# Kernel tuning notes

Measured on AMD Instinct MI355X. Metric: run time of the kernel, lower is better.

Reference implementation:

```python
import jax, jax.numpy as jnp
import numpy as np

ALIGN_SCALE = 3.0
UNIF_SCALE = 1.0
EPS = 1e-12  # torch F.normalize eps


def _normalize(x):
    n = jnp.linalg.norm(x, axis=-1, keepdims=True)
    return x / jnp.maximum(n, EPS)


def _unif_loss(a, b):
    # log(mean(exp(-2 * ||a_i - b_j||^2))) over all N*M pairs, fused via GEMM identity
    sq_a = jnp.sum(a * a, axis=1)  # [N]
    sq_b = jnp.sum(b * b, axis=1)  # [M]
    # squared distances: ||a||^2 + ||b||^2 - 2 a.b, clipped at 0 for numerics
    d2 = jnp.maximum(sq_a[:, None] + sq_b[None, :] - 2.0 * (a @ b.T), 0.0)  # [N, M]
    return jnp.log(jnp.mean(jnp.exp(-2.0 * d2)))


def setup_inputs() -> dict:
    key = jax.random.key(0)
    k1, k2 = jax.random.split(key)
    N, D = 8192, 512
    return {
        "image_embed": jax.random.normal(k1, (N, D), dtype=jnp.float32),
        "text_embed": jax.random.normal(k2, (N, D), dtype=jnp.float32),
    }


def reference(image_embed, text_embed):
    img = _normalize(image_embed)
    txt = _normalize(text_embed)
    # alignment: mean squared L2 between paired embeddings
    diff = img - txt
    align_loss = jnp.mean(jnp.sum(diff * diff, axis=1))
    # single device: gathered-all tensors equal the local tensors
    text_unif = _unif_loss(txt, txt)
    image_unif = _unif_loss(img, img)
    unif_loss = (text_unif + image_unif) / 2.0
    return ALIGN_SCALE * align_loss + UNIF_SCALE * unif_loss
```

## Files before the change

kernel.cpp:

```cpp
#include <hip/hip_runtime.h>
#include <hip/hip_bf16.h>


#define NROWS 8192
#define DBYTES 256
#define NBLK  1056
#define SCALE4 0x7B7B7B7B

typedef __attribute__((ext_vector_type(8)))  int   int8v;
typedef __attribute__((ext_vector_type(4)))  int   int4v;
typedef __attribute__((ext_vector_type(16))) float float16v;

__device__ inline void load_lds16(const void* g, void* l) {
    __builtin_amdgcn_global_load_lds(
        (const __attribute__((address_space(1))) void*)g,
        (__attribute__((address_space(3))) void*)l, 16, 0, 0);
}

__device__ inline int swz(int r) { return (r ^ (r >> 3)) & 7; }

__device__ inline unsigned fp4_code(float x) {
    const float a = fabsf(x);
    unsigned c = (a < 0.25f) ? 0u : (a < 0.75f) ? 1u : (a < 1.25f) ? 2u :
                 (a < 1.75f) ? 3u : (a < 2.5f)  ? 4u : (a < 3.5f)  ? 5u :
                 (a < 5.0f)  ? 6u : 7u;
    return c | ((__float_as_uint(x) >> 28) & 8u);
}

__global__ __launch_bounds__(256) void normalize_kernel(
    const float* __restrict__ img, const float* __restrict__ txt,
    int* __restrict__ nimg, int* __restrict__ ntxt,
    float* __restrict__ alignp,
    float* __restrict__ S)
{
    if (blockIdx.x == 0 && threadIdx.x < 64) S[threadIdx.x] = 0.0f;

    const int lane = threadIdx.x & 63;
    const int wave = threadIdx.x >> 6;
    const int row  = blockIdx.x * 4 + wave;

    const float4* pi = (const float4*)(img + (size_t)row * 512);
    const float4* pt = (const float4*)(txt + (size_t)row * 512);
    const float4 i0 = pi[2 * lane], i1 = pi[2 * lane + 1];
    const float4 t0 = pt[2 * lane], t1 = pt[2 * lane + 1];

    float ssi = i0.x*i0.x + i0.y*i0.y + i0.z*i0.z + i0.w*i0.w
              + i1.x*i1.x + i1.y*i1.y + i1.z*i1.z + i1.w*i1.w;
    float sst = t0.x*t0.x + t0.y*t0.y + t0.z*t0.z + t0.w*t0.w
              + t1.x*t1.x + t1.y*t1.y + t1.z*t1.z + t1.w*t1.w;
    float dot = i0.x*t0.x + i0.y*t0.y + i0.z*t0.z + i0.w*t0.w
              + i1.x*t1.x + i1.y*t1.y + i1.z*t1.z + i1.w*t1.w;

    #pragma unroll
    for (int off = 1; off < 64; off <<= 1) {
        ssi += __shfl_xor(ssi, off);
        sst += __shfl_xor(sst, off);
        dot += __shfl_xor(dot, off);
    }
    const float inv_i = 1.0f / fmaxf(sqrtf(ssi), 1e-12f);
    const float inv_t = 1.0f / fmaxf(sqrtf(sst), 1e-12f);
    const float si = 16.0f * inv_i;
    const float st = 16.0f * inv_t;

    unsigned wi = 0, wt = 0;
    wi |= fp4_code(i0.x * si)       | (fp4_code(i0.y * si) << 4)
       |  (fp4_code(i0.z * si) << 8)| (fp4_code(i0.w * si) << 12)
       |  (fp4_code(i1.x * si) <<16)| (fp4_code(i1.y * si) << 20)
       |  (fp4_code(i1.z * si) <<24)| (fp4_code(i1.w * si) << 28);
    wt |= fp4_code(t0.x * st)       | (fp4_code(t0.y * st) << 4)
       |  (fp4_code(t0.z * st) << 8)| (fp4_code(t0.w * st) << 12)
       |  (fp4_code(t1.x * st) <<16)| (fp4_code(t1.y * st) << 20)
       |  (fp4_code(t1.z * st) <<24)| (fp4_code(t1.w * st) << 28);

    nimg[row * 64 + lane] = (int)wi;
    ntxt[row * 64 + lane] = (int)wt;

    __shared__ float r4[4];
    if (lane == 0) r4[wave] = dot * inv_i * inv_t;
    __syncthreads();
    if (threadIdx.x == 0)
        alignp[blockIdx.x] = r4[0] + r4[1] + r4[2] + r4[3];
}

__global__ __launch_bounds__(512, 2) void gram_kernel(
    const unsigned char* __restrict__ A0,
    const unsigned char* __restrict__ A1,
    float* __restrict__ S)
{
    const int b = blockIdx.x;
    int I = (int)((65.0f - sqrtf(4225.0f - 4.0f * (float)b)) * 0.5f);
    while ((I + 1) * (64 - I) <= b) ++I;
    while (I * (65 - I) > b) --I;
    const int j = 2 * I + (b - I * (65 - I));

    const unsigned char* __restrict__ A = blockIdx.y ? A1 : A0;
    const int tid  = threadIdx.x;
    const int lane = tid & 63;
    const int wave = tid >> 6;
    const int wm = wave & 3;
    const int wn = wave >> 2;
    const int lr = lane & 31;
    const int h  = lane >> 5;

    const unsigned char* gA = A + (size_t)I * 256 * DBYTES;
    const unsigned char* gB = A + (size_t)j * 128 * DBYTES;

    __shared__ __align__(16) unsigned char ldsA[2][256 * 128];
    __shared__ __align__(16) unsigned char ldsB[2][128 * 128];

    float16v acc[2][2];
    #pragma unroll
    for (int a = 0; a < 2; ++a)
        #pragma unroll
        for (int c = 0; c < 2; ++c)
            #pragma unroll
            for (int r = 0; r < 16; ++r) acc[a][c][r] = 0.0f;

    #pragma unroll
    for (int s = 0; s < 2; ++s) {
        const int k0 = s * 128;
        #pragma unroll
        for (int rnd = 0; rnd < 4; ++rnd) {
            const int slot = rnd * 8192 + tid * 16;
            const int r    = slot >> 7;
            const int cp   = (slot >> 4) & 7;
            const int cl   = cp ^ swz(r);
            load_lds16(gA + (size_t)r * DBYTES + k0 + cl * 16, &ldsA[s][slot]);
        }
        #pragma unroll
        for (int rnd = 0; rnd < 2; ++rnd) {
            const int slot = rnd * 8192 + tid * 16;
            const int r    = slot >> 7;
            const int cp   = (slot >> 4) & 7;
            const int cl   = cp ^ swz(r);
            load_lds16(gB + (size_t)r * DBYTES + k0 + cl * 16, &ldsB[s][slot]);
        }
        __builtin_amdgcn_sched_barrier(0);
    }

    asm volatile("s_waitcnt vmcnt(6)" ::: "memory");
    __builtin_amdgcn_sched_barrier(0);
    __builtin_amdgcn_s_barrier();
    __builtin_amdgcn_sched_barrier(0);

    #pragma unroll
    for (int s = 0; s < 2; ++s) {
        #pragma unroll
        for (int kk = 0; kk < 4; ++kk) {
            const int c0 = kk * 2 + h;
            int8v av[2], bv[2];
            #pragma unroll
            for (int mt = 0; mt < 2; ++mt) {
                const int r = wm * 64 + mt * 32 + lr;
                *((int4v*)&av[mt]) =
                    *(const int4v*)&ldsA[s][r * 128 + (c0 ^ swz(r)) * 16];
                *((int4v*)&av[mt] + 1) = (int4v){0, 0, 0, 0};
            }
            #pragma unroll
            for (int nt = 0; nt < 2; ++nt) {
                const int r = wn * 64 + nt * 32 + lr;
                *((int4v*)&bv[nt]) =
                    *(const int4v*)&ldsB[s][r * 128 + (c0 ^ swz(r)) * 16];
                *((int4v*)&bv[nt] + 1) = (int4v){0, 0, 0, 0};
            }
            #pragma unroll
            for (int mt = 0; mt < 2; ++mt)
                #pragma unroll
                for (int nt = 0; nt < 2; ++nt)
                    acc[mt][nt] = __builtin_amdgcn_mfma_scale_f32_32x32x64_f8f6f4(
                        av[mt], bv[nt], acc[mt][nt],
                        4, 4,
                        0, SCALE4,
                        0, SCALE4);
        }
        if (s == 0) {
            asm volatile("s_waitcnt vmcnt(0)" ::: "memory");
            __builtin_amdgcn_s_barrier();
            __builtin_amdgcn_sched_barrier(0);
        }
    }

    const int r128 = 2 * I + (wm >> 1);
    const float wv = (j > r128) ? 2.0f : ((j == r128) ? 1.0f : 0.0f);
    float s = 0.0f;
    #pragma unroll
    for (int mt = 0; mt < 2; ++mt)
        #pragma unroll
        for (int nt = 0; nt < 2; ++nt)
            #pragma unroll
            for (int r2 = 0; r2 < 16; ++r2) {
                const float g = acc[mt][nt][r2];
                s += __expf(4.0f * fminf(g, 1.0f) - 4.0f);
            }
    s *= wv;
    #pragma unroll
    for (int off = 32; off; off >>= 1) s += __shfl_down(s, off);
    __shared__ float ps[8];
    if (lane == 0) ps[wave] = s;
    __syncthreads();
    if (tid == 0) {
        const float tot = ps[0] + ps[1] + ps[2] + ps[3]
                        + ps[4] + ps[5] + ps[6] + ps[7];
        atomicAdd(&S[blockIdx.y * 32 + (blockIdx.x & 31)], tot);
    }
}

__global__ __launch_bounds__(256) void finalize_kernel(
    const float* __restrict__ S,
    const float* __restrict__ alignp,
    float* __restrict__ out)
{
    const int tid = threadIdx.x;
    float a = 0.0f;
    #pragma unroll
    for (int k = 0; k < 8; ++k) a += alignp[tid + 256 * k];
    #pragma unroll
    for (int off = 32; off; off >>= 1) a += __shfl_down(a, off);
    __shared__ float r4[4];
    if ((tid & 63) == 0) r4[tid >> 6] = a;
    __syncthreads();
    if (tid == 0) {
        const double A = (double)r4[0] + r4[1] + r4[2] + r4[3];
        double si = 0.0, st = 0.0;
        for (int k = 0; k < 32; ++k) { si += S[k]; st += S[32 + k]; }
        const double align = 2.0 - 2.0 * A / (double)NROWS;
        const double n2 = (double)NROWS * (double)NROWS;
        const double unif = 0.5 * (log(si / n2) + log(st / n2));
        out[0] = (float)(3.0 * align + unif);
    }
}

extern "C" void kernel_launch(void* const* d_in, const int* in_sizes, int n_in,
                              void* d_out, int out_size, void* d_ws, size_t ws_size,
                              hipStream_t stream) {
    const float* img = (const float*)d_in[0];
    const float* txt = (const float*)d_in[1];
    char* ws = (char*)d_ws;
    int* nimg = (int*)ws;
    int* ntxt = (int*)(ws + (size_t)NROWS * DBYTES);
    float* S      = (float*)(ws + 2 * (size_t)NROWS * DBYTES);
    float* alignp = S + 64;

    normalize_kernel<<<NROWS / 4, 256, 0, stream>>>(img, txt, nimg, ntxt, alignp, S);
    dim3 grid(NBLK, 2);
    gram_kernel<<<grid, 512, 0, stream>>>((const unsigned char*)nimg,
                                          (const unsigned char*)ntxt, S);
    finalize_kernel<<<1, 256, 0, stream>>>(S, alignp, (float*)d_out);
}
```

Baseline: 120.9 us.

## Make gram kernel persistent with 128x128 triangular jobs and double-buffered prefetch

Replaces the 2112-block grid of 256x128 tiles with a persistent grid of 512 blocks of 256 threads. Each block loops over 128x128 upper-triangle jobs from both matrices, with the next K-half staged into LDS while the current one is computed. The diagonal tiles are now exactly triangular, so no half-wasted 256-row strips, and the per-block launch and prologue cost is hidden by the software pipeline. The trade-offs are smaller tiles with less reuse per load, a barrier every stage, and possible load imbalance since jobs don't divide evenly across blocks.

```diff
diff --git a/kernel.cpp b/kernel.cpp
--- a/kernel.cpp
+++ b/kernel.cpp
@@ -4,7 +4,9 @@
 
 #define NROWS 8192
 #define DBYTES 256
-#define NBLK  1056
+#define NTRI  2080
+#define NJOBS 4160
+#define GRAMBLK 512
 #define SCALE4 0x7B7B7B7B
 
 typedef __attribute__((ext_vector_type(8)))  int   int8v;
@@ -82,31 +84,68 @@
         alignp[blockIdx.x] = r4[0] + r4[1] + r4[2] + r4[3];
 }
 
-__global__ __launch_bounds__(512, 2) void gram_kernel(
+__device__ inline void decode_job(int t,
+        const unsigned char* __restrict__ A0,
+        const unsigned char* __restrict__ A1,
+        const unsigned char*& pA, const unsigned char*& pB,
+        float& w0, float& w1)
+{
+    const int m  = (t >= NTRI) ? 1 : 0;
+    const int tt = t - m * NTRI;
+    int i = (int)((129.0f - sqrtf(16641.0f - 8.0f * (float)tt)) * 0.5f);
+    while (64 * (i + 1) - ((i + 1) * i) / 2 <= tt) ++i;
+    while (64 * i - (i * (i - 1)) / 2 > tt) --i;
+    const int j = i + (tt - (64 * i - (i * (i - 1)) / 2));
+    const unsigned char* M = m ? A1 : A0;
+    pA = M + (size_t)i * 128 * DBYTES;
+    pB = M + (size_t)j * 128 * DBYTES;
+    const float w = (j > i) ? 2.0f : 1.0f;
+    w0 = m ? 0.0f : w;
+    w1 = m ? w : 0.0f;
+}
+
+__device__ inline void stage_tile(const unsigned char* __restrict__ pA,
+                                  const unsigned char* __restrict__ pB,
+                                  int k0, unsigned char* lA, unsigned char* lB,
+                                  int tid)
+{
+    #pragma unroll
+    for (int rnd = 0; rnd < 4; ++rnd) {
+        const int slot = rnd * 4096 + tid * 16;
+        const int r    = slot >> 7;
+        const int cp   = (slot >> 4) & 7;
+        const int cl   = cp ^ swz(r);
+        load_lds16(pA + (size_t)r * DBYTES + k0 + cl * 16, lA + slot);
+    }
+    #pragma unroll
+    for (int rnd = 0; rnd < 4; ++rnd) {
+        const int slot = rnd * 4096 + tid * 16;
+        const int r    = slot >> 7;
+        const int cp   = (slot >> 4) & 7;
+        const int cl   = cp ^ swz(r);
+        load_lds16(pB + (size_t)r * DBYTES + k0 + cl * 16, lB + slot);
+    }
+}
+
+__global__ __launch_bounds__(256, 2) void gram_kernel(
     const unsigned char* __restrict__ A0,
     const unsigned char* __restrict__ A1,
     float* __restrict__ S)
 {
-    const int b = blockIdx.x;
-    int I = (int)((65.0f - sqrtf(4225.0f - 4.0f * (float)b)) * 0.5f);
-    while ((I + 1) * (64 - I) <= b) ++I;
-    while (I * (65 - I) > b) --I;
-    const int j = 2 * I + (b - I * (65 - I));
-
-    const unsigned char* __restrict__ A = blockIdx.y ? A1 : A0;
     const int tid  = threadIdx.x;
     const int lane = tid & 63;
     const int wave = tid >> 6;
-    const int wm = wave & 3;
-    const int wn = wave >> 2;
+    const int wm = wave & 1, wn = wave >> 1;
     const int lr = lane & 31;
     const int h  = lane >> 5;
-
-    const unsigned char* gA = A + (size_t)I * 256 * DBYTES;
-    const unsigned char* gB = A + (size_t)j * 128 * DBYTES;
-
-    __shared__ __align__(16) unsigned char ldsA[2][256 * 128];
+    const int b  = blockIdx.x;
+
+    __shared__ __align__(16) unsigned char ldsA[2][128 * 128];
     __shared__ __align__(16) unsigned char ldsB[2][128 * 128];
+    __shared__ float ps[4][2];
+
+    const int J = (NJOBS - 1 - b) / GRAMBLK + 1;
+    const int U = 2 * J;
 
     float16v acc[2][2];
     #pragma unroll
@@ -115,36 +154,31 @@
         for (int c = 0; c < 2; ++c)
             #pragma unroll
             for (int r = 0; r < 16; ++r) acc[a][c][r] = 0.0f;
-
-    #pragma unroll
-    for (int s = 0; s < 2; ++s) {
-        const int k0 = s * 128;
-        #pragma unroll
-        for (int rnd = 0; rnd < 4; ++rnd) {
-            const int slot = rnd * 8192 + tid * 16;
-            const int r    = slot >> 7;
-            const int cp   = (slot >> 4) & 7;
-            const int cl   = cp ^ swz(r);
-            load_lds16(gA + (size_t)r * DBYTES + k0 + cl * 16, &ldsA[s][slot]);
-        }
-        #pragma unroll
-        for (int rnd = 0; rnd < 2; ++rnd) {
-            const int slot = rnd * 8192 + tid * 16;
-            const int r    = slot >> 7;
-            const int cp   = (slot >> 4) & 7;
-            const int cl   = cp ^ swz(r);
-            load_lds16(gB + (size_t)r * DBYTES + k0 + cl * 16, &ldsB[s][slot]);
+    float s0 = 0.0f, s1 = 0.0f;
+
+    const unsigned char *nA, *nB;
+    float nw0, nw1;
+    decode_job(b, A0, A1, nA, nB, nw0, nw1);
+    float cw0 = nw0, cw1 = nw1;
+    stage_tile(nA, nB, 0, ldsA[0], ldsB[0], tid);
+
+    for (int u = 0; u < U; ++u) {
+        const int buf = u & 1;
+        if (u + 1 < U) {
+            const int v = u + 1;
+            if ((v & 1) == 0)
+                decode_job(b + GRAMBLK * (v >> 1), A0, A1, nA, nB, nw0, nw1);
+            stage_tile(nA, nB, (v & 1) * 128, ldsA[v & 1], ldsB[v & 1], tid);
+            asm volatile("s_waitcnt vmcnt(8)" ::: "memory");
+        } else {
+            asm volatile("s_waitcnt vmcnt(0)" ::: "memory");
         }
         __builtin_amdgcn_sched_barrier(0);
-    }
-
-    asm volatile("s_waitcnt vmcnt(6)" ::: "memory");
-    __builtin_amdgcn_sched_barrier(0);
-    __builtin_amdgcn_s_barrier();
-    __builtin_amdgcn_sched_barrier(0);
-
-    #pragma unroll
-    for (int s = 0; s < 2; ++s) {
+        __builtin_amdgcn_s_barrier();
+        __builtin_amdgcn_sched_barrier(0);
+
+        const unsigned char* lA = ldsA[buf];
+        const unsigned char* lB = ldsB[buf];
         #pragma unroll
         for (int kk = 0; kk < 4; ++kk) {
             const int c0 = kk * 2 + h;
@@ -153,14 +187,14 @@
             for (int mt = 0; mt < 2; ++mt) {
                 const int r = wm * 64 + mt * 32 + lr;
                 *((int4v*)&av[mt]) =
-                    *(const int4v*)&ldsA[s][r * 128 + (c0 ^ swz(r)) * 16];
+                    *(const int4v*)&lA[r * 128 + (c0 ^ swz(r)) * 16];
                 *((int4v*)&av[mt] + 1) = (int4v){0, 0, 0, 0};
             }
             #pragma unroll
             for (int nt = 0; nt < 2; ++nt) {
                 const int r = wn * 64 + nt * 32 + lr;
                 *((int4v*)&bv[nt]) =
-                    *(const int4v*)&ldsB[s][r * 128 + (c0 ^ swz(r)) * 16];
+                    *(const int4v*)&lB[r * 128 + (c0 ^ swz(r)) * 16];
                 *((int4v*)&bv[nt] + 1) = (int4v){0, 0, 0, 0};
             }
             #pragma unroll
@@ -173,35 +207,38 @@
                         0, SCALE4,
                         0, SCALE4);
         }
-        if (s == 0) {
-            asm volatile("s_waitcnt vmcnt(0)" ::: "memory");
-            __builtin_amdgcn_s_barrier();
-            __builtin_amdgcn_sched_barrier(0);
+
+        if (u & 1) {
+            float f = 0.0f;
+            #pragma unroll
+            for (int mt = 0; mt < 2; ++mt)
+                #pragma unroll
+                for (int nt = 0; nt < 2; ++nt)
+                    #pragma unroll
+                    for (int r2 = 0; r2 < 16; ++r2) {
+                        const float g = acc[mt][nt][r2];
+                        f += __expf(4.0f * fminf(g, 1.0f) - 4.0f);
+                        acc[mt][nt][r2] = 0.0f;
+                    }
+            s0 += cw0 * f;
+            s1 += cw1 * f;
+            cw0 = nw0;  cw1 = nw1;
         }
-    }
-
-    const int r128 = 2 * I + (wm >> 1);
-    const float wv = (j > r128) ? 2.0f : ((j == r128) ? 1.0f : 0.0f);
-    float s = 0.0f;
-    #pragma unroll
-    for (int mt = 0; mt < 2; ++mt)
-        #pragma unroll
-        for (int nt = 0; nt < 2; ++nt)
-            #pragma unroll
-            for (int r2 = 0; r2 < 16; ++r2) {
-                const float g = acc[mt][nt][r2];
-                s += __expf(4.0f * fminf(g, 1.0f) - 4.0f);
-            }
-    s *= wv;
-    #pragma unroll
-    for (int off = 32; off; off >>= 1) s += __shfl_down(s, off);
-    __shared__ float ps[8];
-    if (lane == 0) ps[wave] = s;
+
+        __builtin_amdgcn_sched_barrier(0);
+        __builtin_amdgcn_s_barrier();
+    }
+
+    #pragma unroll
+    for (int off = 32; off; off >>= 1) {
+        s0 += __shfl_down(s0, off);
+        s1 += __shfl_down(s1, off);
+    }
+    if (lane == 0) { ps[wave][0] = s0; ps[wave][1] = s1; }
     __syncthreads();
     if (tid == 0) {
-        const float tot = ps[0] + ps[1] + ps[2] + ps[3]
-                        + ps[4] + ps[5] + ps[6] + ps[7];
-        atomicAdd(&S[blockIdx.y * 32 + (blockIdx.x & 31)], tot);
+        atomicAdd(&S[b & 31],        ps[0][0] + ps[1][0] + ps[2][0] + ps[3][0]);
+        atomicAdd(&S[32 + (b & 31)], ps[0][1] + ps[1][1] + ps[2][1] + ps[3][1]);
     }
 }
 
@@ -242,8 +279,7 @@
     float* alignp = S + 64;
 
     normalize_kernel<<<NROWS / 4, 256, 0, stream>>>(img, txt, nimg, ntxt, alignp, S);
-    dim3 grid(NBLK, 2);
-    gram_kernel<<<grid, 512, 0, stream>>>((const unsigned char*)nimg,
-                                          (const unsigned char*)ntxt, S);
+    gram_kernel<<<GRAMBLK, 256, 0, stream>>>((const unsigned char*)nimg,
+                                             (const unsigned char*)ntxt, S);
     finalize_kernel<<<1, 256, 0, stream>>>(S, alignp, (float*)d_out);
 }
```

Measured after the change: 115.1 us. 4.8% less time.
